# Kernel tuning notes

Measured on AMD Instinct MI355X. Metric: run time of the kernel, lower is better.

The kernel has to match this reference:

```python
import jax, jax.numpy as jnp
import numpy as np

NUM_USERS = 100000
NUM_RECIPES = 200000
EMB = 32
RDIM = 96
D = EMB + RDIM  # 128, shared node feature dim
E = 1500000
NUM_LAYERS = 3


def setup_inputs() -> dict:
    key = jax.random.key(0)
    k1, k2, k3, k4, k5, k6 = jax.random.split(key, 6)
    usr_emb = 0.1 * jax.random.normal(k1, (NUM_USERS, D), jnp.float32)      # usr_embedding.weight (init std=0.1)
    rcp_emb = 0.1 * jax.random.normal(k2, (NUM_RECIPES, EMB), jnp.float32)  # rcp_embedding.weight
    recipe_feat = jax.random.normal(k3, (NUM_RECIPES, RDIM), jnp.float32)   # x_dict['recipe']
    user_idx = jax.random.randint(k4, (E,), 0, NUM_USERS, jnp.int32)        # edge_index row 0 (user)
    rcp_idx = jax.random.randint(k5, (E,), 0, NUM_RECIPES, jnp.int32)       # edge_index row 1 (recipe)
    edge_weight = 1.0 + 4.0 * jax.random.uniform(k6, (E,), jnp.float32)     # review scores in [1,5]
    return {"usr_emb": usr_emb, "rcp_emb": rcp_emb, "recipe_feat": recipe_feat,
            "edge_weight": edge_weight, "user_idx": user_idx, "rcp_idx": rcp_idx}


def reference(usr_emb, rcp_emb, recipe_feat, edge_weight, user_idx, rcp_idx):
    seg = jax.ops.segment_sum
    alpha = 1.0 / (NUM_LAYERS + 1)

    # LightGCN symmetric normalization with review-score edge weights
    # (HeteroLGConv: msg = x_src[src] * w / sqrt(deg_w(src) * deg_w(dst)); sum-aggregate at dst).
    deg_u = seg(edge_weight, user_idx, num_segments=NUM_USERS)    # weighted user degree
    deg_r = seg(edge_weight, rcp_idx, num_segments=NUM_RECIPES)   # weighted recipe degree
    norm = edge_weight * jax.lax.rsqrt(jnp.clip(deg_u[user_idx] * deg_r[rcp_idx], 1e-12, None))  # [E]

    rcp_x = jnp.concatenate([rcp_emb, recipe_feat], axis=1)  # [R, D]
    usr_x = usr_emb                                           # [U, D]
    rec_out = rcp_x * alpha
    usr_out = usr_x * alpha

    for _ in range(NUM_LAYERS):
        # user -> recipe propagation
        rcp_x = seg(usr_x[user_idx] * norm[:, None], rcp_idx, num_segments=NUM_RECIPES)
        rec_out = rec_out + rcp_x * alpha
        # recipe -> user propagation (reverse edges)
        usr_x = seg(rcp_x[rcp_idx] * norm[:, None], user_idx, num_segments=NUM_USERS)
        usr_out = usr_out + usr_x * alpha

    return usr_out, rec_out
```

## Files before the change

kernel.cpp:

```cpp
#include <hip/hip_runtime.h>
#include <hip/hip_fp16.h>


typedef unsigned long long ull;

constexpr int NU   = 100000;
constexpr int NR   = 200000;
constexpr int EMB  = 32;
constexpr int RDIM = 96;
constexpr int D    = 128;
constexpr int NE   = 1500000;
constexpr float ALPHA = 0.25f;

constexpr ull DEG_MASK = (1ULL << 44) - 1;
constexpr float DEG_SCALE = 1048576.0f;
constexpr float DEG_INV   = 1.0f / 1048576.0f;


__global__ void deg_pack_kernel(const float4* __restrict__ w4,
                                const int4* __restrict__ u4,
                                const int4* __restrict__ r4,
                                ull* __restrict__ pk_u,
                                ull* __restrict__ pk_r,
                                ull* __restrict__ rankp) {
    int i = blockIdx.x * blockDim.x + threadIdx.x;
    if (i < NE / 4) {
        float4 wv = w4[i];
        int4 uu = u4[i];
        int4 rr = r4[i];
        ull v0 = (1ULL << 44) | (ull)(wv.x * DEG_SCALE + 0.5f);
        ull v1 = (1ULL << 44) | (ull)(wv.y * DEG_SCALE + 0.5f);
        ull v2 = (1ULL << 44) | (ull)(wv.z * DEG_SCALE + 0.5f);
        ull v3 = (1ULL << 44) | (ull)(wv.w * DEG_SCALE + 0.5f);
        ull ou0 = atomicAdd(&pk_u[uu.x], v0);
        ull or0 = atomicAdd(&pk_r[rr.x], v0);
        ull ou1 = atomicAdd(&pk_u[uu.y], v1);
        ull or1 = atomicAdd(&pk_r[rr.y], v1);
        ull ou2 = atomicAdd(&pk_u[uu.z], v2);
        ull or2 = atomicAdd(&pk_r[rr.z], v2);
        ull ou3 = atomicAdd(&pk_u[uu.w], v3);
        ull or3 = atomicAdd(&pk_r[rr.w], v3);
        ull pk = ((ou0 >> 44) & 0xFF)        | (((or0 >> 44) & 0xFF) << 8)
               | (((ou1 >> 44) & 0xFF) << 16) | (((or1 >> 44) & 0xFF) << 24)
               | (((ou2 >> 44) & 0xFF) << 32) | (((or2 >> 44) & 0xFF) << 40)
               | (((ou3 >> 44) & 0xFF) << 48) | (((or3 >> 44) & 0xFF) << 56);
        rankp[i] = pk;
    }
}

__global__ void scan_block_both(const ull* __restrict__ pk_r,
                                const ull* __restrict__ pk_u,
                                int* __restrict__ rp_r,
                                int* __restrict__ rp_u,
                                int* __restrict__ bsum, int nbR) {
    __shared__ int tmp[256];
    bool isR = (int)blockIdx.x < nbR;
    const ull* pk = isR ? pk_r : pk_u;
    int* excl = isR ? rp_r : rp_u;
    int ncnt  = isR ? NR : NU;
    int b     = isR ? (int)blockIdx.x : (int)blockIdx.x - nbR;
    int nscan = ncnt + 1;
    int i = b * 256 + threadIdx.x;
    int v = 0;
    if (i < ncnt) v = ((int)(pk[i] >> 44) + 7) & ~7;
    tmp[threadIdx.x] = v;
    __syncthreads();
    for (int off = 1; off < 256; off <<= 1) {
        int t = (threadIdx.x >= off) ? tmp[threadIdx.x - off] : 0;
        __syncthreads();
        tmp[threadIdx.x] += t;
        __syncthreads();
    }
    if (i < nscan) excl[i] = tmp[threadIdx.x] - v;
    if (threadIdx.x == 255) bsum[blockIdx.x] = tmp[255];
}

__global__ void scan_bsum2(int* __restrict__ bsum, int nbR, int nbU) {
    __shared__ int tmp[1024];
    int off = (blockIdx.x == 0) ? 0 : nbR;
    int nb  = (blockIdx.x == 0) ? nbR : nbU;
    int i = threadIdx.x;
    int v = (i < nb) ? bsum[off + i] : 0;
    tmp[i] = v;
    __syncthreads();
    for (int o = 1; o < 1024; o <<= 1) {
        int t = (i >= o) ? tmp[i - o] : 0;
        __syncthreads();
        tmp[i] += t;
        __syncthreads();
    }
    if (i < nb) bsum[off + i] = tmp[i] - v;
}

__global__ void scan_add_both(int* __restrict__ rp_r, int* __restrict__ rp_u,
                              const int* __restrict__ bsum, int nbR) {
    bool isR = (int)blockIdx.x < nbR;
    int* excl = isR ? rp_r : rp_u;
    int ncnt  = isR ? NR : NU;
    int b     = isR ? (int)blockIdx.x : (int)blockIdx.x - nbR;
    int i = b * 256 + threadIdx.x;
    if (i < ncnt + 1) excl[i] += bsum[blockIdx.x];
}

__global__ void fill_kernel(const float4* __restrict__ w4,
                            const int4* __restrict__ u4,
                            const int4* __restrict__ r4,
                            const ull* __restrict__ pk_u,
                            const ull* __restrict__ pk_r,
                            const int* __restrict__ rp_u,
                            const int* __restrict__ rp_r,
                            const ull* __restrict__ rankp,
                            unsigned* __restrict__ pair_u,
                            unsigned* __restrict__ pair_r) {
    int i = blockIdx.x * blockDim.x + threadIdx.x;
    if (i >= NE / 4) return;
    float4 wv = w4[i];
    int4 uu = u4[i];
    int4 rr = r4[i];
    ull rk = rankp[i];

#define FILL_ONE(WW, U, R, SH)                                               \
    {                                                                        \
        int u = (U), r = (R);                                                \
        float du = (float)(pk_u[u] & DEG_MASK) * DEG_INV;                    \
        float dr = (float)(pk_r[r] & DEG_MASK) * DEG_INV;                    \
        float nv = (WW) * rsqrtf(fmaxf(du * dr, 1e-12f));                    \
        unsigned short hb = __half_as_ushort(__float2half(nv));              \
        unsigned n14 = ((unsigned)hb + 1u) >> 1;                             \
        int rku = (int)((rk >> (SH)) & 0xFF);                                \
        int rkr = (int)((rk >> ((SH) + 8)) & 0xFF);                          \
        pair_r[rp_r[r] + rkr] = (n14 << 18) | (unsigned)u;                   \
        pair_u[rp_u[u] + rku] = (n14 << 18) | (unsigned)r;                   \
    }

    FILL_ONE(wv.x, uu.x, rr.x, 0)
    FILL_ONE(wv.y, uu.y, rr.y, 16)
    FILL_ONE(wv.z, uu.z, rr.z, 32)
    FILL_ONE(wv.w, uu.w, rr.w, 48)
#undef FILL_ONE
}


__device__ __forceinline__ unsigned pack_bf16x2(float x, float y) {
    unsigned ux = __float_as_uint(x);
    unsigned uy = __float_as_uint(y);
    ux += 0x7fffu + ((ux >> 16) & 1u);
    uy += 0x7fffu + ((uy >> 16) & 1u);
    return (ux >> 16) | (uy & 0xffff0000u);
}

__device__ __forceinline__ float blo(unsigned u) { return __uint_as_float(u << 16); }
__device__ __forceinline__ float bhi(unsigned u) { return __uint_as_float(u & 0xffff0000u); }

__global__ void to_bf16_kernel(const float* __restrict__ in,
                               unsigned* __restrict__ out, int n) {
    int i = blockIdx.x * blockDim.x + threadIdx.x;
    if (i < n) {
        float2 v = reinterpret_cast<const float2*>(in)[i];
        out[i] = pack_bf16x2(v.x, v.y);
    }
}

__global__ void gather_rows(const unsigned* __restrict__ src,
                            const int* __restrict__ rp,
                            const unsigned* __restrict__ pair,
                            unsigned* __restrict__ xout,
                            float* __restrict__ out_f,
                            const unsigned* __restrict__ prev1,
                            const unsigned* __restrict__ prev2,
                            const float* __restrict__ init_a,
                            const float* __restrict__ init_b,
                            int nrows) {
    int wid  = (blockIdx.x * blockDim.x + threadIdx.x) >> 6;
    wid = __builtin_amdgcn_readfirstlane(wid);
    int lane = threadIdx.x & 63;
    if (wid >= nrows) return;

    int beg = __builtin_amdgcn_readfirstlane(rp[wid]);
    int end = __builtin_amdgcn_readfirstlane(rp[wid + 1]);
    float x0 = 0.f, y0 = 0.f, x1 = 0.f, y1 = 0.f;
    float x2 = 0.f, y2 = 0.f, x3 = 0.f, y3 = 0.f;

#define LOAD_EDGE(P, AX, AY)                                                  \
    {                                                                         \
        unsigned s = (P) & 0x3FFFFu;                                          \
        float n = __half2float(__ushort_as_half(                              \
                      (unsigned short)(((P) >> 18) << 1)));                   \
        unsigned v = src[(size_t)s * 64 + lane];                              \
        AX += n * __uint_as_float(v << 16);                                   \
        AY += n * __uint_as_float(v & 0xffff0000u);                           \
    }

    for (int e = beg; e < end; e += 8) {
        uint4 pa = *reinterpret_cast<const uint4*>(pair + e);
        uint4 pb = *reinterpret_cast<const uint4*>(pair + e + 4);
        LOAD_EDGE(pa.x, x0, y0)
        LOAD_EDGE(pa.y, x1, y1)
        LOAD_EDGE(pa.z, x2, y2)
        LOAD_EDGE(pa.w, x3, y3)
        LOAD_EDGE(pb.x, x0, y0)
        LOAD_EDGE(pb.y, x1, y1)
        LOAD_EDGE(pb.z, x2, y2)
        LOAD_EDGE(pb.w, x3, y3)
    }
#undef LOAD_EDGE

    x0 = (x0 + x1) + (x2 + x3);
    y0 = (y0 + y1) + (y2 + y3);

    size_t xo = (size_t)wid * 64 + lane;
    if (xout) xout[xo] = pack_bf16x2(x0, y0);

    if (out_f) {
        size_t o = (size_t)wid * D + lane * 2;
        if (prev1) {
            float2 b;
            if (init_b) {
                b = (lane < 16)
                    ? *reinterpret_cast<const float2*>(init_a + (size_t)wid * EMB + lane * 2)
                    : *reinterpret_cast<const float2*>(init_b + (size_t)wid * RDIM + (lane * 2 - EMB));
            } else {
                b = *reinterpret_cast<const float2*>(init_a + o);
            }
            unsigned v1 = prev1[xo], v2 = prev2[xo];
            float lo = b.x + blo(v1) + blo(v2) + x0;
            float hi = b.y + bhi(v1) + bhi(v2) + y0;
            float2 ov = {ALPHA * lo, ALPHA * hi};
            *reinterpret_cast<float2*>(out_f + o) = ov;
        } else if (init_a) {
            float2 b;
            if (init_b) {
                b = (lane < 16)
                    ? *reinterpret_cast<const float2*>(init_a + (size_t)wid * EMB + lane * 2)
                    : *reinterpret_cast<const float2*>(init_b + (size_t)wid * RDIM + (lane * 2 - EMB));
            } else {
                b = *reinterpret_cast<const float2*>(init_a + o);
            }
            float2 ov = {ALPHA * (b.x + x0), ALPHA * (b.y + y0)};
            *reinterpret_cast<float2*>(out_f + o) = ov;
        } else {
            float2 ov = *reinterpret_cast<float2*>(out_f + o);
            ov.x += ALPHA * x0; ov.y += ALPHA * y0;
            *reinterpret_cast<float2*>(out_f + o) = ov;
        }
    }
}


extern "C" void kernel_launch(void* const* d_in, const int* in_sizes, int n_in,
                              void* d_out, int out_size, void* d_ws, size_t ws_size,
                              hipStream_t stream) {
    const float* usr_emb = (const float*)d_in[0];
    const float* rcp_emb = (const float*)d_in[1];
    const float* rfeat   = (const float*)d_in[2];
    const float* w       = (const float*)d_in[3];
    const int*   ui      = (const int*)d_in[4];
    const int*   ri      = (const int*)d_in[5];

    float* out     = (float*)d_out;
    float* usr_out = out;
    float* rec_out = out + (size_t)NU * D;

    char* p0 = (char*)d_ws;
    char* p = p0;
    auto take = [&](size_t bytes) -> char* {
        char* q = p;
        p += (bytes + 255) & ~(size_t)255;
        return q;
    };

    const int PR_SLOTS = NE + 7 * NR;
    const int PU_SLOTS = NE + 7 * NU;

    ull*      pk_u   = (ull*)take((size_t)NU * 8);
    ull*      pk_r   = (ull*)take((size_t)NR * 8);
    unsigned* pair_r = (unsigned*)take((size_t)PR_SLOTS * 4);
    unsigned* pair_u = (unsigned*)take((size_t)PU_SLOTS * 4);
    char*     zero_end = p;
    ull*      rankp = (ull*)take((size_t)(NE / 4) * 8);
    int*      rp_r  = (int*)take((size_t)(NR + 1) * 4);
    int*      rp_u  = (int*)take((size_t)(NU + 1) * 4);
    int*      bsum  = (int*)take(4096 * 4);
    unsigned* emb_h = (unsigned*)take((size_t)NU * 64 * 4);

    const size_t xr_b = (size_t)NR * 64 * 4;
    const size_t xu_b = (size_t)NU * 64 * 4;
    size_t used_head = (size_t)(p - p0);
    bool deferred = (ws_size >= used_head + 3 * ((xr_b + 255) & ~(size_t)255)
                                         + 2 * ((xu_b + 255) & ~(size_t)255));

    unsigned *xr0, *xr1, *xr2, *xu0, *xu1;
    if (deferred) {
        xr0 = (unsigned*)take(xr_b); xr1 = (unsigned*)take(xr_b); xr2 = (unsigned*)take(xr_b);
        xu0 = (unsigned*)take(xu_b); xu1 = (unsigned*)take(xu_b);
    } else {
        xr0 = xr1 = xr2 = (unsigned*)take(xr_b);
        xu0 = xu1 = (unsigned*)take(xu_b);
    }

    const int B = 256;
    const int QB = (NE / 4 + B - 1) / B;

    hipMemsetAsync(pk_u, 0, (size_t)(zero_end - (char*)pk_u), stream);

    to_bf16_kernel<<<(NU * 64 + B - 1) / B, B, 0, stream>>>(usr_emb, emb_h, NU * 64);
    deg_pack_kernel<<<QB, B, 0, stream>>>((const float4*)w, (const int4*)ui,
                                          (const int4*)ri, pk_u, pk_r, rankp);

    const int nbR = (NR + 1 + 255) / 256;
    const int nbU = (NU + 1 + 255) / 256;
    scan_block_both<<<nbR + nbU, 256, 0, stream>>>(pk_r, pk_u, rp_r, rp_u, bsum, nbR);
    scan_bsum2<<<2, 1024, 0, stream>>>(bsum, nbR, nbU);
    scan_add_both<<<nbR + nbU, 256, 0, stream>>>(rp_r, rp_u, bsum, nbR);

    fill_kernel<<<QB, B, 0, stream>>>((const float4*)w, (const int4*)ui,
                                      (const int4*)ri, pk_u, pk_r, rp_u, rp_r,
                                      rankp, pair_u, pair_r);

    const int GB_R = (NR * 64 + B - 1) / B;
    const int GB_U = (NU * 64 + B - 1) / B;

    if (deferred) {
        gather_rows<<<GB_R, B, 0, stream>>>(emb_h, rp_r, pair_r, xr0,
                                            nullptr, nullptr, nullptr, nullptr, nullptr, NR);
        gather_rows<<<GB_U, B, 0, stream>>>(xr0, rp_u, pair_u, xu0,
                                            nullptr, nullptr, nullptr, nullptr, nullptr, NU);
        gather_rows<<<GB_R, B, 0, stream>>>(xu0, rp_r, pair_r, xr1,
                                            nullptr, nullptr, nullptr, nullptr, nullptr, NR);
        gather_rows<<<GB_U, B, 0, stream>>>(xr1, rp_u, pair_u, xu1,
                                            nullptr, nullptr, nullptr, nullptr, nullptr, NU);
        gather_rows<<<GB_R, B, 0, stream>>>(xu1, rp_r, pair_r, xr2,
                                            rec_out, xr0, xr1, rcp_emb, rfeat, NR);
        gather_rows<<<GB_U, B, 0, stream>>>(xr2, rp_u, pair_u, nullptr,
                                            usr_out, xu0, xu1, usr_emb, nullptr, NU);
    } else {
        gather_rows<<<GB_R, B, 0, stream>>>(emb_h, rp_r, pair_r, xr0,
                                            rec_out, nullptr, nullptr, rcp_emb, rfeat, NR);
        gather_rows<<<GB_U, B, 0, stream>>>(xr0, rp_u, pair_u, xu0,
                                            usr_out, nullptr, nullptr, usr_emb, nullptr, NU);
        gather_rows<<<GB_R, B, 0, stream>>>(xu0, rp_r, pair_r, xr0,
                                            rec_out, nullptr, nullptr, nullptr, nullptr, NR);
        gather_rows<<<GB_U, B, 0, stream>>>(xr0, rp_u, pair_u, xu0,
                                            usr_out, nullptr, nullptr, nullptr, nullptr, NU);
        gather_rows<<<GB_R, B, 0, stream>>>(xu0, rp_r, pair_r, xr0,
                                            rec_out, nullptr, nullptr, nullptr, nullptr, NR);
        gather_rows<<<GB_U, B, 0, stream>>>(xr0, rp_u, pair_u, nullptr,
                                            usr_out, nullptr, nullptr, nullptr, nullptr, NU);
    }
}
```

Measured before the change: 637.0 us.

## Fuse bf16 conversion into degree kernel, pack offsets with degrees, unroll gather

Merges the user-embedding bf16 conversion into the degree/rank atomic kernel as extra blocks, which saves one launch. The scan-add pass now also writes a combined int2 of row offset and float degree, so the fill kernel does one 8-byte lookup per endpoint instead of separate offset and packed-degree reads. The main gather loop is unrolled to 16 edges per iteration, with the pair buffers padded by 16 slots. The non-deferred fallback path gets a separate init kernel and a simpler accumulate kernel. The int2 arrays add memory traffic in the finalize step.

```diff
diff --git a/kernel.cpp b/kernel.cpp
--- a/kernel.cpp
+++ b/kernel.cpp
@@ -16,13 +16,43 @@
 constexpr float DEG_SCALE = 1048576.0f;
 constexpr float DEG_INV   = 1.0f / 1048576.0f;
 
-
-__global__ void deg_pack_kernel(const float4* __restrict__ w4,
+constexpr int QB = (NE / 4 + 255) / 256;
+constexpr int CB = (NU * D / 16 + 255) / 256;
+
+
+__device__ __forceinline__ unsigned pack_bf16x2(float x, float y) {
+    unsigned ux = __float_as_uint(x);
+    unsigned uy = __float_as_uint(y);
+    ux += 0x7fffu + ((ux >> 16) & 1u);
+    uy += 0x7fffu + ((uy >> 16) & 1u);
+    return (ux >> 16) | (uy & 0xffff0000u);
+}
+
+__device__ __forceinline__ float blo(unsigned u) { return __uint_as_float(u << 16); }
+__device__ __forceinline__ float bhi(unsigned u) { return __uint_as_float(u & 0xffff0000u); }
+
+
+__global__ void deg_bf16_kernel(const float4* __restrict__ w4,
                                 const int4* __restrict__ u4,
                                 const int4* __restrict__ r4,
                                 ull* __restrict__ pk_u,
                                 ull* __restrict__ pk_r,
-                                ull* __restrict__ rankp) {
+                                ull* __restrict__ rankp,
+                                const float4* __restrict__ usr_emb4,
+                                uint4* __restrict__ emb_h4) {
+    if ((int)blockIdx.x >= QB) {
+        int t = ((int)blockIdx.x - QB) * 256 + threadIdx.x;
+        int base = t * 4;
+        float4 a = usr_emb4[base], b = usr_emb4[base + 1];
+        float4 c = usr_emb4[base + 2], d = usr_emb4[base + 3];
+        uint4 o0 = {pack_bf16x2(a.x, a.y), pack_bf16x2(a.z, a.w),
+                    pack_bf16x2(b.x, b.y), pack_bf16x2(b.z, b.w)};
+        uint4 o1 = {pack_bf16x2(c.x, c.y), pack_bf16x2(c.z, c.w),
+                    pack_bf16x2(d.x, d.y), pack_bf16x2(d.z, d.w)};
+        emb_h4[t * 2]     = o0;
+        emb_h4[t * 2 + 1] = o1;
+        return;
+    }
     int i = blockIdx.x * blockDim.x + threadIdx.x;
     if (i < NE / 4) {
         float4 wv = w4[i];
@@ -40,13 +70,14 @@
         ull or2 = atomicAdd(&pk_r[rr.z], v2);
         ull ou3 = atomicAdd(&pk_u[uu.w], v3);
         ull or3 = atomicAdd(&pk_r[rr.w], v3);
-        ull pk = ((ou0 >> 44) & 0xFF)        | (((or0 >> 44) & 0xFF) << 8)
+        ull pk = ((ou0 >> 44) & 0xFF)         | (((or0 >> 44) & 0xFF) << 8)
                | (((ou1 >> 44) & 0xFF) << 16) | (((or1 >> 44) & 0xFF) << 24)
                | (((ou2 >> 44) & 0xFF) << 32) | (((or2 >> 44) & 0xFF) << 40)
                | (((ou3 >> 44) & 0xFF) << 48) | (((or3 >> 44) & 0xFF) << 56);
         rankp[i] = pk;
     }
 }
+
 
 __global__ void scan_block_both(const ull* __restrict__ pk_r,
                                 const ull* __restrict__ pk_u,
@@ -92,23 +123,33 @@
     if (i < nb) bsum[off + i] = tmp[i] - v;
 }
 
-__global__ void scan_add_both(int* __restrict__ rp_r, int* __restrict__ rp_u,
+__global__ void finalize_both(const int* __restrict__ rp_r,
+                              const int* __restrict__ rp_u,
+                              const ull* __restrict__ pk_r,
+                              const ull* __restrict__ pk_u,
+                              int2* __restrict__ combo_r,
+                              int2* __restrict__ combo_u,
                               const int* __restrict__ bsum, int nbR) {
     bool isR = (int)blockIdx.x < nbR;
-    int* excl = isR ? rp_r : rp_u;
+    const int* rp = isR ? rp_r : rp_u;
+    const ull* pk = isR ? pk_r : pk_u;
+    int2* combo   = isR ? combo_r : combo_u;
     int ncnt  = isR ? NR : NU;
     int b     = isR ? (int)blockIdx.x : (int)blockIdx.x - nbR;
     int i = b * 256 + threadIdx.x;
-    if (i < ncnt + 1) excl[i] += bsum[blockIdx.x];
-}
+    if (i < ncnt + 1) {
+        int rpv = rp[i] + bsum[blockIdx.x];
+        float deg = (i < ncnt) ? (float)(pk[i] & DEG_MASK) * DEG_INV : 0.0f;
+        combo[i] = make_int2(rpv, __float_as_int(deg));
+    }
+}
+
 
 __global__ void fill_kernel(const float4* __restrict__ w4,
                             const int4* __restrict__ u4,
                             const int4* __restrict__ r4,
-                            const ull* __restrict__ pk_u,
-                            const ull* __restrict__ pk_r,
-                            const int* __restrict__ rp_u,
-                            const int* __restrict__ rp_r,
+                            const int2* __restrict__ combo_u,
+                            const int2* __restrict__ combo_r,
                             const ull* __restrict__ rankp,
                             unsigned* __restrict__ pair_u,
                             unsigned* __restrict__ pair_r) {
@@ -121,16 +162,17 @@
 
 #define FILL_ONE(WW, U, R, SH)                                               \
     {                                                                        \
-        int u = (U), r = (R);                                                \
-        float du = (float)(pk_u[u] & DEG_MASK) * DEG_INV;                    \
-        float dr = (float)(pk_r[r] & DEG_MASK) * DEG_INV;                    \
+        int2 cu = combo_u[(U)];                                              \
+        int2 cr = combo_r[(R)];                                              \
+        float du = __int_as_float(cu.y);                                     \
+        float dr = __int_as_float(cr.y);                                     \
         float nv = (WW) * rsqrtf(fmaxf(du * dr, 1e-12f));                    \
         unsigned short hb = __half_as_ushort(__float2half(nv));              \
         unsigned n14 = ((unsigned)hb + 1u) >> 1;                             \
         int rku = (int)((rk >> (SH)) & 0xFF);                                \
         int rkr = (int)((rk >> ((SH) + 8)) & 0xFF);                          \
-        pair_r[rp_r[r] + rkr] = (n14 << 18) | (unsigned)u;                   \
-        pair_u[rp_u[u] + rku] = (n14 << 18) | (unsigned)r;                   \
+        pair_r[cr.x + rkr] = (n14 << 18) | (unsigned)(U);                    \
+        pair_u[cu.x + rku] = (n14 << 18) | (unsigned)(R);                    \
     }
 
     FILL_ONE(wv.x, uu.x, rr.x, 0)
@@ -140,29 +182,8 @@
 #undef FILL_ONE
 }
 
-
-__device__ __forceinline__ unsigned pack_bf16x2(float x, float y) {
-    unsigned ux = __float_as_uint(x);
-    unsigned uy = __float_as_uint(y);
-    ux += 0x7fffu + ((ux >> 16) & 1u);
-    uy += 0x7fffu + ((uy >> 16) & 1u);
-    return (ux >> 16) | (uy & 0xffff0000u);
-}
-
-__device__ __forceinline__ float blo(unsigned u) { return __uint_as_float(u << 16); }
-__device__ __forceinline__ float bhi(unsigned u) { return __uint_as_float(u & 0xffff0000u); }
-
-__global__ void to_bf16_kernel(const float* __restrict__ in,
-                               unsigned* __restrict__ out, int n) {
-    int i = blockIdx.x * blockDim.x + threadIdx.x;
-    if (i < n) {
-        float2 v = reinterpret_cast<const float2*>(in)[i];
-        out[i] = pack_bf16x2(v.x, v.y);
-    }
-}
-
 __global__ void gather_rows(const unsigned* __restrict__ src,
-                            const int* __restrict__ rp,
+                            const int2* __restrict__ combo,
                             const unsigned* __restrict__ pair,
                             unsigned* __restrict__ xout,
                             float* __restrict__ out_f,
@@ -176,8 +197,8 @@
     int lane = threadIdx.x & 63;
     if (wid >= nrows) return;
 
-    int beg = __builtin_amdgcn_readfirstlane(rp[wid]);
-    int end = __builtin_amdgcn_readfirstlane(rp[wid + 1]);
+    int beg = __builtin_amdgcn_readfirstlane(combo[wid].x);
+    int end = __builtin_amdgcn_readfirstlane(combo[wid + 1].x);
     float x0 = 0.f, y0 = 0.f, x1 = 0.f, y1 = 0.f;
     float x2 = 0.f, y2 = 0.f, x3 = 0.f, y3 = 0.f;
 
@@ -191,17 +212,28 @@
         AY += n * __uint_as_float(v & 0xffff0000u);                           \
     }
 
-    for (int e = beg; e < end; e += 8) {
+    int e = beg;
+    for (; e + 16 <= end; e += 16) {
         uint4 pa = *reinterpret_cast<const uint4*>(pair + e);
         uint4 pb = *reinterpret_cast<const uint4*>(pair + e + 4);
-        LOAD_EDGE(pa.x, x0, y0)
-        LOAD_EDGE(pa.y, x1, y1)
-        LOAD_EDGE(pa.z, x2, y2)
-        LOAD_EDGE(pa.w, x3, y3)
-        LOAD_EDGE(pb.x, x0, y0)
-        LOAD_EDGE(pb.y, x1, y1)
-        LOAD_EDGE(pb.z, x2, y2)
-        LOAD_EDGE(pb.w, x3, y3)
+        uint4 pc = *reinterpret_cast<const uint4*>(pair + e + 8);
+        uint4 pd = *reinterpret_cast<const uint4*>(pair + e + 12);
+        LOAD_EDGE(pa.x, x0, y0) LOAD_EDGE(pa.y, x1, y1)
+        LOAD_EDGE(pa.z, x2, y2) LOAD_EDGE(pa.w, x3, y3)
+        LOAD_EDGE(pb.x, x0, y0) LOAD_EDGE(pb.y, x1, y1)
+        LOAD_EDGE(pb.z, x2, y2) LOAD_EDGE(pb.w, x3, y3)
+        LOAD_EDGE(pc.x, x0, y0) LOAD_EDGE(pc.y, x1, y1)
+        LOAD_EDGE(pc.z, x2, y2) LOAD_EDGE(pc.w, x3, y3)
+        LOAD_EDGE(pd.x, x0, y0) LOAD_EDGE(pd.y, x1, y1)
+        LOAD_EDGE(pd.z, x2, y2) LOAD_EDGE(pd.w, x3, y3)
+    }
+    for (; e < end; e += 8) {
+        uint4 pa = *reinterpret_cast<const uint4*>(pair + e);
+        uint4 pb = *reinterpret_cast<const uint4*>(pair + e + 4);
+        LOAD_EDGE(pa.x, x0, y0) LOAD_EDGE(pa.y, x1, y1)
+        LOAD_EDGE(pa.z, x2, y2) LOAD_EDGE(pa.w, x3, y3)
+        LOAD_EDGE(pb.x, x0, y0) LOAD_EDGE(pb.y, x1, y1)
+        LOAD_EDGE(pb.z, x2, y2) LOAD_EDGE(pb.w, x3, y3)
     }
 #undef LOAD_EDGE
 
@@ -213,36 +245,71 @@
 
     if (out_f) {
         size_t o = (size_t)wid * D + lane * 2;
+        float2 b;
+        if (init_b) {
+            b = (lane < 16)
+                ? *reinterpret_cast<const float2*>(init_a + (size_t)wid * EMB + lane * 2)
+                : *reinterpret_cast<const float2*>(init_b + (size_t)wid * RDIM + (lane * 2 - EMB));
+        } else {
+            b = *reinterpret_cast<const float2*>(init_a + o);
+        }
         if (prev1) {
-            float2 b;
-            if (init_b) {
-                b = (lane < 16)
-                    ? *reinterpret_cast<const float2*>(init_a + (size_t)wid * EMB + lane * 2)
-                    : *reinterpret_cast<const float2*>(init_b + (size_t)wid * RDIM + (lane * 2 - EMB));
-            } else {
-                b = *reinterpret_cast<const float2*>(init_a + o);
-            }
             unsigned v1 = prev1[xo], v2 = prev2[xo];
             float lo = b.x + blo(v1) + blo(v2) + x0;
             float hi = b.y + bhi(v1) + bhi(v2) + y0;
             float2 ov = {ALPHA * lo, ALPHA * hi};
             *reinterpret_cast<float2*>(out_f + o) = ov;
-        } else if (init_a) {
-            float2 b;
-            if (init_b) {
-                b = (lane < 16)
-                    ? *reinterpret_cast<const float2*>(init_a + (size_t)wid * EMB + lane * 2)
-                    : *reinterpret_cast<const float2*>(init_b + (size_t)wid * RDIM + (lane * 2 - EMB));
-            } else {
-                b = *reinterpret_cast<const float2*>(init_a + o);
-            }
+        } else {
             float2 ov = {ALPHA * (b.x + x0), ALPHA * (b.y + y0)};
             *reinterpret_cast<float2*>(out_f + o) = ov;
-        } else {
-            float2 ov = *reinterpret_cast<float2*>(out_f + o);
-            ov.x += ALPHA * x0; ov.y += ALPHA * y0;
-            *reinterpret_cast<float2*>(out_f + o) = ov;
         }
+    }
+}
+
+__global__ void gather_rows_acc(const unsigned* __restrict__ src,
+                                const int2* __restrict__ combo,
+                                const unsigned* __restrict__ pair,
+                                unsigned* __restrict__ xout,
+                                float* __restrict__ out_f,
+                                int nrows) {
+    int wid  = (blockIdx.x * blockDim.x + threadIdx.x) >> 6;
+    wid = __builtin_amdgcn_readfirstlane(wid);
+    int lane = threadIdx.x & 63;
+    if (wid >= nrows) return;
+    int beg = __builtin_amdgcn_readfirstlane(combo[wid].x);
+    int end = __builtin_amdgcn_readfirstlane(combo[wid + 1].x);
+    float x0 = 0.f, y0 = 0.f;
+    for (int e = beg; e < end; ++e) {
+        unsigned P = pair[e];
+        unsigned s = P & 0x3FFFFu;
+        float n = __half2float(__ushort_as_half((unsigned short)((P >> 18) << 1)));
+        unsigned v = src[(size_t)s * 64 + lane];
+        x0 += n * blo(v); y0 += n * bhi(v);
+    }
+    size_t xo = (size_t)wid * 64 + lane;
+    if (xout) xout[xo] = pack_bf16x2(x0, y0);
+    size_t o = (size_t)wid * D + lane * 2;
+    float2 ov = *reinterpret_cast<float2*>(out_f + o);
+    ov.x += ALPHA * x0; ov.y += ALPHA * y0;
+    *reinterpret_cast<float2*>(out_f + o) = ov;
+}
+
+__global__ void init_out_kernel(const float* __restrict__ usr_emb,
+                                const float* __restrict__ rcp_emb,
+                                const float* __restrict__ rfeat,
+                                float* __restrict__ out) {
+    long long i = blockIdx.x * (long long)blockDim.x + threadIdx.x;
+    const long long UD = (long long)NU * D;
+    const long long RD = (long long)NR * D;
+    if (i < UD) {
+        out[i] = ALPHA * usr_emb[i];
+    } else if (i < UD + RD) {
+        long long j = i - UD;
+        int r = (int)(j >> 7);
+        int d = (int)(j & 127);
+        float v = (d < EMB) ? rcp_emb[(long long)r * EMB + d]
+                            : rfeat[(long long)r * RDIM + (d - EMB)];
+        out[i] = ALPHA * v;
     }
 }
 
@@ -269,19 +336,21 @@
         return q;
     };
 
-    const int PR_SLOTS = NE + 7 * NR;
-    const int PU_SLOTS = NE + 7 * NU;
+    const int PR_SLOTS = NE + 7 * NR + 16;
+    const int PU_SLOTS = NE + 7 * NU + 16;
 
     ull*      pk_u   = (ull*)take((size_t)NU * 8);
     ull*      pk_r   = (ull*)take((size_t)NR * 8);
     unsigned* pair_r = (unsigned*)take((size_t)PR_SLOTS * 4);
     unsigned* pair_u = (unsigned*)take((size_t)PU_SLOTS * 4);
     char*     zero_end = p;
-    ull*      rankp = (ull*)take((size_t)(NE / 4) * 8);
-    int*      rp_r  = (int*)take((size_t)(NR + 1) * 4);
-    int*      rp_u  = (int*)take((size_t)(NU + 1) * 4);
-    int*      bsum  = (int*)take(4096 * 4);
-    unsigned* emb_h = (unsigned*)take((size_t)NU * 64 * 4);
+    ull*      rankp   = (ull*)take((size_t)(NE / 4) * 8);
+    int*      rp_r    = (int*)take((size_t)(NR + 1) * 4);
+    int*      rp_u    = (int*)take((size_t)(NU + 1) * 4);
+    int2*     combo_r = (int2*)take((size_t)(NR + 1) * 8);
+    int2*     combo_u = (int2*)take((size_t)(NU + 1) * 8);
+    int*      bsum    = (int*)take(4096 * 4);
+    unsigned* emb_h   = (unsigned*)take((size_t)NU * 64 * 4);
 
     const size_t xr_b = (size_t)NR * 64 * 4;
     const size_t xu_b = (size_t)NU * 64 * 4;
@@ -299,52 +368,48 @@
     }
 
     const int B = 256;
-    const int QB = (NE / 4 + B - 1) / B;
 
     hipMemsetAsync(pk_u, 0, (size_t)(zero_end - (char*)pk_u), stream);
 
-    to_bf16_kernel<<<(NU * 64 + B - 1) / B, B, 0, stream>>>(usr_emb, emb_h, NU * 64);
-    deg_pack_kernel<<<QB, B, 0, stream>>>((const float4*)w, (const int4*)ui,
-                                          (const int4*)ri, pk_u, pk_r, rankp);
+    deg_bf16_kernel<<<QB + CB, B, 0, stream>>>(
+        (const float4*)w, (const int4*)ui, (const int4*)ri,
+        pk_u, pk_r, rankp, (const float4*)usr_emb, (uint4*)emb_h);
 
     const int nbR = (NR + 1 + 255) / 256;
     const int nbU = (NU + 1 + 255) / 256;
     scan_block_both<<<nbR + nbU, 256, 0, stream>>>(pk_r, pk_u, rp_r, rp_u, bsum, nbR);
     scan_bsum2<<<2, 1024, 0, stream>>>(bsum, nbR, nbU);
-    scan_add_both<<<nbR + nbU, 256, 0, stream>>>(rp_r, rp_u, bsum, nbR);
+    finalize_both<<<nbR + nbU, 256, 0, stream>>>(rp_r, rp_u, pk_r, pk_u,
+                                                 combo_r, combo_u, bsum, nbR);
 
     fill_kernel<<<QB, B, 0, stream>>>((const float4*)w, (const int4*)ui,
-                                      (const int4*)ri, pk_u, pk_r, rp_u, rp_r,
+                                      (const int4*)ri, combo_u, combo_r,
                                       rankp, pair_u, pair_r);
 
     const int GB_R = (NR * 64 + B - 1) / B;
     const int GB_U = (NU * 64 + B - 1) / B;
 
     if (deferred) {
-        gather_rows<<<GB_R, B, 0, stream>>>(emb_h, rp_r, pair_r, xr0,
+        gather_rows<<<GB_R, B, 0, stream>>>(emb_h, combo_r, pair_r, xr0,
                                             nullptr, nullptr, nullptr, nullptr, nullptr, NR);
-        gather_rows<<<GB_U, B, 0, stream>>>(xr0, rp_u, pair_u, xu0,
+        gather_rows<<<GB_U, B, 0, stream>>>(xr0, combo_u, pair_u, xu0,
                                             nullptr, nullptr, nullptr, nullptr, nullptr, NU);
-        gather_rows<<<GB_R, B, 0, stream>>>(xu0, rp_r, pair_r, xr1,
+        gather_rows<<<GB_R, B, 0, stream>>>(xu0, combo_r, pair_r, xr1,
                                             nullptr, nullptr, nullptr, nullptr, nullptr, NR);
-        gather_rows<<<GB_U, B, 0, stream>>>(xr1, rp_u, pair_u, xu1,
+        gather_rows<<<GB_U, B, 0, stream>>>(xr1, combo_u, pair_u, xu1,
                                             nullptr, nullptr, nullptr, nullptr, nullptr, NU);
-        gather_rows<<<GB_R, B, 0, stream>>>(xu1, rp_r, pair_r, xr2,
+        gather_rows<<<GB_R, B, 0, stream>>>(xu1, combo_r, pair_r, xr2,
                                             rec_out, xr0, xr1, rcp_emb, rfeat, NR);
-        gather_rows<<<GB_U, B, 0, stream>>>(xr2, rp_u, pair_u, nullptr,
+        gather_rows<<<GB_U, B, 0, stream>>>(xr2, combo_u, pair_u, nullptr,
                                             usr_out, xu0, xu1, usr_emb, nullptr, NU);
     } else {
-        gather_rows<<<GB_R, B, 0, stream>>>(emb_h, rp_r, pair_r, xr0,
-                                            rec_out, nullptr, nullptr, rcp_emb, rfeat, NR);
-        gather_rows<<<GB_U, B, 0, stream>>>(xr0, rp_u, pair_u, xu0,
-                                            usr_out, nullptr, nullptr, usr_emb, nullptr, NU);
-        gather_rows<<<GB_R, B, 0, stream>>>(xu0, rp_r, pair_r, xr0,
-                                            rec_out, nullptr, nullptr, nullptr, nullptr, NR);
-        gather_rows<<<GB_U, B, 0, stream>>>(xr0, rp_u, pair_u, xu0,
-                                            usr_out, nullptr, nullptr, nullptr, nullptr, NU);
-        gather_rows<<<GB_R, B, 0, stream>>>(xu0, rp_r, pair_r, xr0,
-                                            rec_out, nullptr, nullptr, nullptr, nullptr, NR);
-        gather_rows<<<GB_U, B, 0, stream>>>(xr0, rp_u, pair_u, nullptr,
-                                            usr_out, nullptr, nullptr, nullptr, nullptr, NU);
-    }
-}
+        long long tot = (long long)(NU + NR) * D;
+        init_out_kernel<<<(int)((tot + B - 1) / B), B, 0, stream>>>(usr_emb, rcp_emb, rfeat, out);
+        gather_rows_acc<<<GB_R, B, 0, stream>>>(emb_h, combo_r, pair_r, xr0, rec_out, NR);
+        gather_rows_acc<<<GB_U, B, 0, stream>>>(xr0, combo_u, pair_u, xu0, usr_out, NU);
+        gather_rows_acc<<<GB_R, B, 0, stream>>>(xu0, combo_r, pair_r, xr0, rec_out, NR);
+        gather_rows_acc<<<GB_U, B, 0, stream>>>(xr0, combo_u, pair_u, xu0, usr_out, NU);
+        gather_rows_acc<<<GB_R, B, 0, stream>>>(xu0, combo_r, pair_r, xr0, rec_out, NR);
+        gather_rows_acc<<<GB_U, B, 0, stream>>>(xr0, combo_u, pair_u, nullptr, usr_out, NU);
+    }
+}
```

After: 614.4 us. 1.04x faster.
